# Kernel tuning notes

Hardware: AMD Instinct MI355X
Metric: run time of the kernel (lower is better)

## Reference

```python
import jax, jax.numpy as jnp
import numpy as np

H = 128          # input spatial size forced by hardcoded reshape (8 * 16)
BATCH = 128
BLK = 8          # block_size
SUB = 16         # out_channels (sub-frames)
WIN = 3          # window


def setup_inputs() -> dict:
    key = jax.random.key(0)
    k1, k2 = jax.random.split(key, 2)
    coded = jax.random.normal(k1, (BATCH, 1, H, H), dtype=jnp.float32)
    # Conv3d weight: [out=16*64, in/groups=1, kD=9, 1, 1]; kaiming-like scale sqrt(2/9)
    weight = jax.random.normal(k2, (SUB * BLK * BLK, 1, WIN * WIN, 1, 1), dtype=jnp.float32) * np.sqrt(2.0 / 9.0).astype(np.float32)
    bias = jnp.zeros((SUB * BLK * BLK,), dtype=jnp.float32)
    return {"coded": coded, "weight": weight, "bias": bias}


def reference(coded, weight, bias):
    N = coded.shape[0]
    # --- window_shuffle: conv with 3x3 identity filters, pad 1 == 9 shifted copies ---
    pad = jnp.pad(coded, ((0, 0), (0, 0), (1, 1), (1, 1)))  # [N,1,H+2,H+2]
    patches = jnp.stack(
        [pad[:, 0, i:i + H, j:j + H] for i in range(WIN) for j in range(WIN)],
        axis=1,
    )  # [N,9,H,H]
    # --- reverse_pixel_shuffle (space-to-depth, block 8), vectorized over the 9 channels ---
    Hs = H // BLK  # 16
    x = patches.reshape(N, WIN * WIN, Hs, BLK, Hs, BLK)
    x = x.transpose(0, 1, 3, 5, 2, 4).reshape(N, WIN * WIN, BLK * BLK, Hs, Hs)
    x = x.transpose(0, 2, 1, 3, 4)  # [N,64,9,16,16] (torch.stack dim=2 order)
    # --- depthwise Conv3d: groups=64, kernel (9,1,1) -> per-group 9-tap dot ---
    W = weight.reshape(BLK * BLK, SUB, WIN * WIN)  # [64,16,9]
    b = bias.reshape(BLK * BLK, SUB)               # [64,16]
    out = jnp.einsum('ngihw,gmi->ngmhw', x, W) + b[None, :, :, None, None]  # [N,64,16,16,16]
    # --- reshape/transpose/pixel-shuffle ---
    out = out.transpose(0, 2, 1, 3, 4).reshape(N, SUB * BLK * BLK, Hs, Hs)  # [N,1024,16,16]
    out = out.reshape(N, SUB, BLK, BLK, Hs, Hs)
    out = out.transpose(0, 1, 4, 2, 5, 3).reshape(N, SUB, H, H)  # [N,16,128,128]
    return out
```

## Files before the change

### kernel.cpp

```cpp
#include <hip/hip_runtime.h>


#define H 128
#define N_BATCH 128
#define SUB 16

__global__ void wprep_kernel(const float* __restrict__ w,
                             const float* __restrict__ bias,
                             float* __restrict__ Wt) {
    int t = blockIdx.x * blockDim.x + threadIdx.x;
    if (t >= 8 * 16 * 8) return;
    int b1 = t >> 7;
    int m  = (t >> 3) & 15;
    int j  = t & 7;
    int h  = j >> 2;
    int jj = j & 3;
    int oc = (b1 * 8 + j) * 16 + m;
    float* dst = Wt + (b1 * 16 + m) * 80 + h * 40;
#pragma unroll
    for (int i = 0; i < 9; ++i) dst[i * 4 + jj] = w[oc * 9 + i];
    dst[36 + jj] = bias[oc];
}

__global__ __launch_bounds__(256, 8) void shiftconv_kernel(
        const float* __restrict__ x,
        const float* __restrict__ Wt,
        float* __restrict__ out) {
    int bid = blockIdx.x;
    int nlo = bid & 7;
    int q   = bid >> 3;
    int mh  = q & 1;
    int rh  = (q >> 1) & 1;
    int b1  = (q >> 2) & 7;
    int n   = ((q >> 5) << 3) | nlo;

    __shared__ float ws[8 * 80];
    {
        int t = threadIdx.x;
        if (t < 160)
            ((float4*)ws)[t] = ((const float4*)(Wt + (b1 * 16 + mh * 8) * 80))[t];
    }

    int c  = threadIdx.x & 31;
    int r8 = threadIdx.x >> 5;
    int y  = b1 + (rh << 6) + (r8 << 3);
    int x0 = c << 2;
    int h  = c & 1;

    const float* xn = x + (size_t)n * (H * H);

    float in[3][6];
#pragma unroll
    for (int dy = 0; dy < 3; ++dy) {
        int ry = y + dy - 1;
        float4 a = make_float4(0.0f, 0.0f, 0.0f, 0.0f);
        if (ry >= 0 && ry < H) a = *(const float4*)(xn + ry * H + x0);
        in[dy][1] = a.x; in[dy][2] = a.y; in[dy][3] = a.z; in[dy][4] = a.w;
        float left  = __shfl_up(a.w, 1);
        float right = __shfl_down(a.x, 1);
        in[dy][0] = (c == 0)  ? 0.0f : left;
        in[dy][5] = (c == 31) ? 0.0f : right;
    }

    __syncthreads();

    float* outbase = out + ((size_t)(n * SUB + mh * 8)) * (H * H) + y * H + x0;

#pragma unroll
    for (int mi = 0; mi < 8; ++mi) {
        const float4* wp = (const float4*)(ws + mi * 80 + h * 40);
        float4 b4 = wp[9];
        float acc[4] = {b4.x, b4.y, b4.z, b4.w};
#pragma unroll
        for (int dy = 0; dy < 3; ++dy) {
#pragma unroll
            for (int dj = 0; dj < 3; ++dj) {
                float4 w4 = wp[dy * 3 + dj];
                acc[0] = fmaf(in[dy][dj + 0], w4.x, acc[0]);
                acc[1] = fmaf(in[dy][dj + 1], w4.y, acc[1]);
                acc[2] = fmaf(in[dy][dj + 2], w4.z, acc[2]);
                acc[3] = fmaf(in[dy][dj + 3], w4.w, acc[3]);
            }
        }
        *(float4*)(outbase + (size_t)mi * (H * H)) =
            make_float4(acc[0], acc[1], acc[2], acc[3]);
    }
}

extern "C" void kernel_launch(void* const* d_in, const int* in_sizes, int n_in,
                              void* d_out, int out_size, void* d_ws, size_t ws_size,
                              hipStream_t stream) {
    const float* coded  = (const float*)d_in[0];
    const float* weight = (const float*)d_in[1];
    const float* bias   = (const float*)d_in[2];
    float* out = (float*)d_out;
    float* Wt  = (float*)d_ws;

    wprep_kernel<<<4, 256, 0, stream>>>(weight, bias, Wt);
    shiftconv_kernel<<<N_BATCH * 8 * 2 * 2, 256, 0, stream>>>(coded, Wt, out);
}
```

Baseline: 147.4 us.

## Fuse weight prep into conv kernel and compute two row groups per thread

Drops the separate weight-transpose kernel and has each block gather its own weights and bias from the raw tensors into shared memory, saving one launch and a workspace round-trip. Each thread now computes two output rows 64 apart, reusing the shared weights across both, which halves the grid size. Occupancy hint drops from 8 to 4, and register pressure grows with the doubled input and accumulator arrays. The in-block weight gather uses scattered, uncoalesced loads.

```diff
diff --git a/kernel.cpp b/kernel.cpp
--- a/kernel.cpp
+++ b/kernel.cpp
@@ -5,85 +5,88 @@
 #define N_BATCH 128
 #define SUB 16
 
-__global__ void wprep_kernel(const float* __restrict__ w,
-                             const float* __restrict__ bias,
-                             float* __restrict__ Wt) {
-    int t = blockIdx.x * blockDim.x + threadIdx.x;
-    if (t >= 8 * 16 * 8) return;
-    int b1 = t >> 7;
-    int m  = (t >> 3) & 15;
-    int j  = t & 7;
-    int h  = j >> 2;
-    int jj = j & 3;
-    int oc = (b1 * 8 + j) * 16 + m;
-    float* dst = Wt + (b1 * 16 + m) * 80 + h * 40;
-#pragma unroll
-    for (int i = 0; i < 9; ++i) dst[i * 4 + jj] = w[oc * 9 + i];
-    dst[36 + jj] = bias[oc];
-}
-
-__global__ __launch_bounds__(256, 8) void shiftconv_kernel(
+__global__ __launch_bounds__(256, 4) void shiftconv_kernel(
         const float* __restrict__ x,
-        const float* __restrict__ Wt,
+        const float* __restrict__ w,
+        const float* __restrict__ bias,
         float* __restrict__ out) {
     int bid = blockIdx.x;
     int nlo = bid & 7;
     int q   = bid >> 3;
     int mh  = q & 1;
-    int rh  = (q >> 1) & 1;
-    int b1  = (q >> 2) & 7;
-    int n   = ((q >> 5) << 3) | nlo;
+    int b1  = (q >> 1) & 7;
+    int n   = ((q >> 4) << 3) | nlo;
 
     __shared__ float ws[8 * 80];
     {
         int t = threadIdx.x;
-        if (t < 160)
-            ((float4*)ws)[t] = ((const float4*)(Wt + (b1 * 16 + mh * 8) * 80))[t];
+        if (t < 64) {
+            int mi = t >> 3;
+            int h  = (t >> 2) & 1;
+            int jj = t & 3;
+            int oc = (b1 * 8 + 4 * h + jj) * 16 + (mh * 8 + mi);
+            float* dst = ws + mi * 80 + h * 40;
+            const float* src = w + oc * 9;
+#pragma unroll
+            for (int i = 0; i < 9; ++i) dst[i * 4 + jj] = src[i];
+            dst[36 + jj] = bias[oc];
+        }
     }
 
     int c  = threadIdx.x & 31;
-    int r8 = threadIdx.x >> 5;
-    int y  = b1 + (rh << 6) + (r8 << 3);
+    int r  = threadIdx.x >> 5;
     int x0 = c << 2;
     int h  = c & 1;
+    int y0 = b1 + (r << 3);
 
     const float* xn = x + (size_t)n * (H * H);
 
-    float in[3][6];
+    float in[2][3][6];
 #pragma unroll
-    for (int dy = 0; dy < 3; ++dy) {
-        int ry = y + dy - 1;
-        float4 a = make_float4(0.0f, 0.0f, 0.0f, 0.0f);
-        if (ry >= 0 && ry < H) a = *(const float4*)(xn + ry * H + x0);
-        in[dy][1] = a.x; in[dy][2] = a.y; in[dy][3] = a.z; in[dy][4] = a.w;
-        float left  = __shfl_up(a.w, 1);
-        float right = __shfl_down(a.x, 1);
-        in[dy][0] = (c == 0)  ? 0.0f : left;
-        in[dy][5] = (c == 31) ? 0.0f : right;
+    for (int g = 0; g < 2; ++g) {
+        int yg = y0 + (g << 6);
+#pragma unroll
+        for (int dy = 0; dy < 3; ++dy) {
+            int ry = yg + dy - 1;
+            float4 a = make_float4(0.0f, 0.0f, 0.0f, 0.0f);
+            if (ry >= 0 && ry < H) a = *(const float4*)(xn + ry * H + x0);
+            in[g][dy][1] = a.x; in[g][dy][2] = a.y;
+            in[g][dy][3] = a.z; in[g][dy][4] = a.w;
+            float left  = __shfl_up(a.w, 1);
+            float right = __shfl_down(a.x, 1);
+            in[g][dy][0] = (c == 0)  ? 0.0f : left;
+            in[g][dy][5] = (c == 31) ? 0.0f : right;
+        }
     }
 
     __syncthreads();
 
-    float* outbase = out + ((size_t)(n * SUB + mh * 8)) * (H * H) + y * H + x0;
+    float* ob = out + ((size_t)(n * SUB + mh * 8)) * (H * H) + y0 * H + x0;
 
 #pragma unroll
     for (int mi = 0; mi < 8; ++mi) {
         const float4* wp = (const float4*)(ws + mi * 80 + h * 40);
         float4 b4 = wp[9];
-        float acc[4] = {b4.x, b4.y, b4.z, b4.w};
+        float a0[4] = {b4.x, b4.y, b4.z, b4.w};
+        float a1[4] = {b4.x, b4.y, b4.z, b4.w};
 #pragma unroll
         for (int dy = 0; dy < 3; ++dy) {
 #pragma unroll
             for (int dj = 0; dj < 3; ++dj) {
                 float4 w4 = wp[dy * 3 + dj];
-                acc[0] = fmaf(in[dy][dj + 0], w4.x, acc[0]);
-                acc[1] = fmaf(in[dy][dj + 1], w4.y, acc[1]);
-                acc[2] = fmaf(in[dy][dj + 2], w4.z, acc[2]);
-                acc[3] = fmaf(in[dy][dj + 3], w4.w, acc[3]);
+                a0[0] = fmaf(in[0][dy][dj + 0], w4.x, a0[0]);
+                a0[1] = fmaf(in[0][dy][dj + 1], w4.y, a0[1]);
+                a0[2] = fmaf(in[0][dy][dj + 2], w4.z, a0[2]);
+                a0[3] = fmaf(in[0][dy][dj + 3], w4.w, a0[3]);
+                a1[0] = fmaf(in[1][dy][dj + 0], w4.x, a1[0]);
+                a1[1] = fmaf(in[1][dy][dj + 1], w4.y, a1[1]);
+                a1[2] = fmaf(in[1][dy][dj + 2], w4.z, a1[2]);
+                a1[3] = fmaf(in[1][dy][dj + 3], w4.w, a1[3]);
             }
         }
-        *(float4*)(outbase + (size_t)mi * (H * H)) =
-            make_float4(acc[0], acc[1], acc[2], acc[3]);
+        float* p = ob + (size_t)mi * (H * H);
+        *(float4*)(p)          = make_float4(a0[0], a0[1], a0[2], a0[3]);
+        *(float4*)(p + 64 * H) = make_float4(a1[0], a1[1], a1[2], a1[3]);
     }
 }
 
@@ -94,8 +97,6 @@
     const float* weight = (const float*)d_in[1];
     const float* bias   = (const float*)d_in[2];
     float* out = (float*)d_out;
-    float* Wt  = (float*)d_ws;
 
-    wprep_kernel<<<4, 256, 0, stream>>>(weight, bias, Wt);
-    shiftconv_kernel<<<N_BATCH * 8 * 2 * 2, 256, 0, stream>>>(coded, Wt, out);
+    shiftconv_kernel<<<N_BATCH * 8 * 2, 256, 0, stream>>>(coded, weight, bias, out);
 }
```

Result: no change. 146.1 us (-0.9%).
